# Kernel tuning notes

Measured on AMD Instinct MI355X. Metric: run time of the kernel, lower is better.

The kernel has to match this reference:

```python
import jax, jax.numpy as jnp
import numpy as np


def setup_inputs() -> dict:
    key = jax.random.key(0)
    ks = jax.random.split(key, 8)
    N, E, H, C, L, G = 100000, 1600000, 128, 10, 5, 64
    x = jax.random.normal(ks[0], (N, H), dtype=jnp.float32)
    edge_index = jax.random.randint(ks[1], (2, E), 0, N, dtype=jnp.int32)
    batch = jnp.sort(jax.random.randint(ks[2], (N,), 0, G, dtype=jnp.int32))
    # Glorot-ish init scale for stability
    Ws = jax.random.normal(ks[3], (L, H, H), dtype=jnp.float32) * (1.0 / np.sqrt(H))
    bs = jax.random.normal(ks[4], (L, H), dtype=jnp.float32) * 0.01
    W_out = jax.random.normal(ks[5], (H, C), dtype=jnp.float32) * (1.0 / np.sqrt(H))
    b_out = jax.random.normal(ks[6], (C,), dtype=jnp.float32) * 0.01
    return {"x": x, "edge_index": edge_index, "batch": batch, "num_graphs": G,
            "Ws": Ws, "bs": bs, "W_out": W_out, "b_out": b_out}


def reference(x, edge_index, batch, num_graphs, Ws, bs, W_out, b_out):
    N = x.shape[0]
    # --- GCN normalization (add self-loops, symmetric deg^-1/2 norm), computed once ---
    loop = jnp.arange(N, dtype=edge_index.dtype)
    src = jnp.concatenate([edge_index[0], loop])  # message sources (x_j)
    dst = jnp.concatenate([edge_index[1], loop])  # aggregation targets
    deg = jax.ops.segment_sum(jnp.ones_like(dst, dtype=x.dtype), dst, num_segments=N)
    dis = jnp.where(deg > 0, jax.lax.rsqrt(jnp.maximum(deg, 1.0)), 0.0)
    norm = dis[src] * dis[dst]  # [E+N]
    # --- stacked GCNConv + ReLU ---
    for l in range(Ws.shape[0]):
        xw = x @ Ws[l]                                   # [N, H] dense transform
        msg = norm[:, None] * xw[src]                    # gather + scale per edge
        x = jax.nn.relu(jax.ops.segment_sum(msg, dst, num_segments=N) + bs[l])
    # --- global mean pool over graphs ---
    sums = jax.ops.segment_sum(x, batch, num_segments=num_graphs)       # [G, H]
    cnts = jax.ops.segment_sum(jnp.ones((N,), x.dtype), batch, num_segments=num_graphs)
    pooled = sums / jnp.maximum(cnts, 1.0)[:, None]
    return pooled @ W_out + b_out
```

## Files before the change

kernel.cpp:

```cpp
#include <hip/hip_runtime.h>
#include <hip/hip_bf16.h>
#include <stdint.h>

#define HDIM 128

typedef __attribute__((ext_vector_type(8))) short short8;
typedef __attribute__((ext_vector_type(4))) float f32x4;

__device__ __forceinline__ ushort f2bf(float f) {
  uint u = __float_as_uint(f);
  u = (u + 0x7fffu + ((u >> 16) & 1u)) >> 16;
  return (ushort)u;
}
__device__ __forceinline__ float bflo(uint v) { return __uint_as_float(v << 16); }
__device__ __forceinline__ float bfhi(uint v) { return __uint_as_float(v & 0xffff0000u); }


__global__ __launch_bounds__(256) void bucket_edges(const int* __restrict__ ei,
                                                    int* __restrict__ cnt,
                                                    int* __restrict__ bktcur,
                                                    int2* __restrict__ bkt, int E,
                                                    float inv8, int cap) {
  __shared__ int hist[8], base[8];
  const int t = threadIdx.x;
  for (int i0 = blockIdx.x * 256; i0 < E; i0 += gridDim.x * 256) {
    int i = i0 + t;
    if (t < 8) hist[t] = 0;
    __syncthreads();
    int s = 0, d = 0, b = 0, rank = 0;
    bool valid = i < E;
    if (valid) {
      s = ei[i];
      d = ei[E + i];
      atomicAdd(&cnt[d], 1);
      b = min(7, (int)((float)d * inv8));
      rank = atomicAdd(&hist[b], 1);
    }
    __syncthreads();
    if (t < 8) base[t] = atomicAdd(&bktcur[t], hist[t]);
    __syncthreads();
    if (valid) bkt[(size_t)b * cap + base[b] + rank] = make_int2(s, d);
  }
}

__global__ __launch_bounds__(256) void dis_kernel(const int* __restrict__ cnt,
                                                  float* __restrict__ dis, int N) {
  int i = blockIdx.x * 256 + threadIdx.x;
  if (i < N) dis[i] = rsqrtf((float)(cnt[i] + 1));
}

__device__ __forceinline__ int pdeg4(int c) { return (c + 4) & ~3; }

__global__ __launch_bounds__(256) void scan1(const int* __restrict__ cnt,
                                             int* __restrict__ bsum, int N) {
  __shared__ int red[256];
  int b = blockIdx.x, t = threadIdx.x;
  int base = b * 1024;
  int s = 0;
  for (int i = t; i < 1024; i += 256) {
    int n = base + i;
    if (n < N) s += pdeg4(cnt[n]);
  }
  red[t] = s;
  __syncthreads();
  for (int off = 128; off; off >>= 1) {
    if (t < off) red[t] += red[t + off];
    __syncthreads();
  }
  if (t == 0) bsum[b] = red[0];
}

__global__ __launch_bounds__(256) void scan2(int* __restrict__ bsum, int nb) {
  __shared__ int sh[256];
  int t = threadIdx.x;
  int v = (t < nb) ? bsum[t] : 0;
  sh[t] = v;
  __syncthreads();
  for (int off = 1; off < 256; off <<= 1) {
    int add = (t >= off) ? sh[t - off] : 0;
    __syncthreads();
    sh[t] += add;
    __syncthreads();
  }
  if (t < nb) bsum[t] = sh[t] - v;
}

__global__ __launch_bounds__(256) void scan3(const int* __restrict__ cnt,
                                             const int* __restrict__ bsum,
                                             int* __restrict__ rowptr,
                                             int* __restrict__ cursor, int N) {
  __shared__ int sh[256];
  int b = blockIdx.x, t = threadIdx.x;
  int base = b * 1024 + t * 4;
  int v[4];
#pragma unroll
  for (int i = 0; i < 4; ++i) {
    int n = base + i;
    v[i] = (n < N) ? pdeg4(cnt[n]) : 0;
  }
  int tsum = v[0] + v[1] + v[2] + v[3];
  sh[t] = tsum;
  __syncthreads();
  for (int off = 1; off < 256; off <<= 1) {
    int add = (t >= off) ? sh[t - off] : 0;
    __syncthreads();
    sh[t] += add;
    __syncthreads();
  }
  int p = sh[t] - tsum + bsum[b];
#pragma unroll
  for (int i = 0; i < 4; ++i) {
    int n = base + i;
    if (n <= N) rowptr[n] = p;
    if (n < N) cursor[n] = p;
    p += v[i];
  }
}

__device__ __forceinline__ uint pack_cw(int src, float w) {
  uint w15 = (__float_as_uint(w) + 0x8000u) >> 16;
  return (uint)src | (w15 << 17);
}
__device__ __forceinline__ uint cw_src(uint u) { return u & 0x1FFFFu; }
__device__ __forceinline__ float cw_w(uint u) { return __uint_as_float((u >> 17) << 16); }

__global__ __launch_bounds__(256) void fill_csr2(const int2* __restrict__ bkt,
                                                 const int* __restrict__ bktcnt,
                                                 const float* __restrict__ dis,
                                                 int* __restrict__ cursor,
                                                 uint* __restrict__ colw, int cap,
                                                 int E, int N) {
  const int g = blockIdx.x & 7;
  const int nb = gridDim.x >> 3;
  const int bi = blockIdx.x >> 3;
  const int ecnt = bktcnt[g];
  const int2* eb = bkt + (size_t)g * cap;
  for (int i = bi * 256 + threadIdx.x; i < ecnt; i += nb * 256) {
    int2 sd = eb[i];
    int pos = atomicAdd(&cursor[sd.y], 1);
    colw[pos] = pack_cw(sd.x, dis[sd.x] * dis[sd.y]);
  }
  const int n0 = (g * N) >> 3, n1 = ((g + 1) * N) >> 3;
  for (int n = n0 + bi * 256 + threadIdx.x; n < n1; n += nb * 256) {
    int pos = atomicAdd(&cursor[n], 1);
    colw[pos] = pack_cw(n, dis[n] * dis[n]);
  }
}

__global__ __launch_bounds__(256) void pad_csr2(const int* __restrict__ cnt,
                                                const int* __restrict__ rowptr,
                                                uint* __restrict__ colw, int N) {
  const int g = blockIdx.x & 7;
  const int nb = gridDim.x >> 3;
  const int bi = blockIdx.x >> 3;
  const int n0 = (g * N) >> 3, n1 = ((g + 1) * N) >> 3;
  for (int n = n0 + bi * 256 + threadIdx.x; n < n1; n += nb * 256) {
    int beg = rowptr[n] + cnt[n] + 1, end = rowptr[n + 1];
    for (int j = beg; j < end; ++j) colw[j] = (uint)n;
  }
}

__global__ __launch_bounds__(256) void swz_w(const float* __restrict__ Ws,
                                             ushort* __restrict__ Wsw, int total) {
  int idx = blockIdx.x * 256 + threadIdx.x;
  if (idx >= total) return;
  int l = idx >> 14, r = idx & 16383;
  int j = r & 7, lane = (r >> 3) & 63, kk = (r >> 9) & 3, c = r >> 11;
  int n = c * 16 + (lane & 15);
  int k = kk * 32 + (lane >> 4) * 8 + j;
  Wsw[idx] = f2bf(Ws[l * 16384 + k * HDIM + n]);
}


template <bool F32IN>
__global__ __launch_bounds__(256) void gemm_kernel(const void* __restrict__ Xin,
                                                   const ushort* __restrict__ Wsw,
                                                   ushort* __restrict__ XW, int N,
                                                   int ntiles) {
  __shared__ ushort wlds[16384];
  __shared__ ushort clds[64 * 136];
  const int t = threadIdx.x;
  {
    const int4* src = (const int4*)Wsw;
    int4* dst = (int4*)wlds;
#pragma unroll
    for (int i = 0; i < 8; ++i) dst[t + 256 * i] = src[t + 256 * i];
  }
  __syncthreads();

  const int wave = t >> 6, lane = t & 63;
  const int kq = lane >> 4;

  for (int tile = blockIdx.x; tile < ntiles; tile += gridDim.x) {
    const int row0 = tile * 64 + wave * 16 + (lane & 15);
    const bool inb = row0 < N;

    short8 afr[4];
#pragma unroll
    for (int kk = 0; kk < 4; ++kk) afr[kk] = short8{0, 0, 0, 0, 0, 0, 0, 0};
    if (inb) {
      if constexpr (F32IN) {
        const float* arow = (const float*)Xin + (size_t)row0 * HDIM;
#pragma unroll
        for (int kk = 0; kk < 4; ++kk) {
          float4 x0 = *(const float4*)(arow + kk * 32 + kq * 8);
          float4 x1 = *(const float4*)(arow + kk * 32 + kq * 8 + 4);
          short8 f;
          f[0] = (short)f2bf(x0.x); f[1] = (short)f2bf(x0.y);
          f[2] = (short)f2bf(x0.z); f[3] = (short)f2bf(x0.w);
          f[4] = (short)f2bf(x1.x); f[5] = (short)f2bf(x1.y);
          f[6] = (short)f2bf(x1.z); f[7] = (short)f2bf(x1.w);
          afr[kk] = f;
        }
      } else {
        const short8* arow = (const short8*)((const ushort*)Xin + (size_t)row0 * HDIM);
#pragma unroll
        for (int kk = 0; kk < 4; ++kk) afr[kk] = arow[kk * 4 + kq];
      }
    }

    f32x4 acc[8];
#pragma unroll
    for (int c = 0; c < 8; ++c) acc[c] = f32x4{0.f, 0.f, 0.f, 0.f};
#pragma unroll
    for (int kk = 0; kk < 4; ++kk) {
#pragma unroll
      for (int c = 0; c < 8; ++c) {
        short8 bfr = *(const short8*)(wlds + (((c * 4 + kk) * 64 + lane) << 3));
        acc[c] = __builtin_amdgcn_mfma_f32_16x16x32_bf16(afr[kk], bfr, acc[c], 0, 0, 0);
      }
    }

    __syncthreads();
    const int m0 = wave * 16 + kq * 4;
#pragma unroll
    for (int c = 0; c < 8; ++c) {
      int col = c * 16 + (lane & 15);
#pragma unroll
      for (int r = 0; r < 4; ++r) clds[(m0 + r) * 136 + col] = f2bf(acc[c][r]);
    }
    __syncthreads();
#pragma unroll
    for (int i = 0; i < 4; ++i) {
      int idx = t + 256 * i;
      int row = idx >> 4, piece = idx & 15;
      int grow = tile * 64 + row;
      if (grow < N)
        ((int4*)XW)[(size_t)tile * 1024 + idx] =
            *(const int4*)(clds + row * 136 + piece * 8);
    }
  }
}

__global__ __launch_bounds__(256, 6) void agg_kernel(const ushort* __restrict__ XW,
                                                     const uint* __restrict__ colw,
                                                     const int* __restrict__ rowptr,
                                                     const float* __restrict__ bias,
                                                     ushort* __restrict__ Y, int N) {
  const int lane = threadIdx.x & 63;
  const int node = blockIdx.x * 4 + (threadIdx.x >> 6);
  if (node >= N) return;
  const int e = lane >> 4, c = lane & 15;
  const int beg = rowptr[node];
  const int pdeg = rowptr[node + 1] - beg;
  const int last = pdeg - 1;

  uint cw[6];
#pragma unroll
  for (int k = 0; k < 6; ++k) {
    int off = 4 * k + e;
    cw[k] = __builtin_nontemporal_load(colw + beg + (off < pdeg ? off : last));
  }
  uint4 gv[6];
#pragma unroll
  for (int k = 0; k < 6; ++k)
    gv[k] = *(const uint4*)(XW + ((size_t)cw_src(cw[k]) << 7) + c * 8);

  float acc[8];
#pragma unroll
  for (int i = 0; i < 8; ++i) acc[i] = 0.f;

#pragma unroll
  for (int k = 0; k < 6; ++k) {
    int off = 4 * k + e;
    float w = (off < pdeg) ? cw_w(cw[k]) : 0.f;
    uint4 v = gv[k];
    acc[0] += w * bflo(v.x); acc[1] += w * bfhi(v.x);
    acc[2] += w * bflo(v.y); acc[3] += w * bfhi(v.y);
    acc[4] += w * bflo(v.z); acc[5] += w * bfhi(v.z);
    acc[6] += w * bflo(v.w); acc[7] += w * bfhi(v.w);
  }
  for (int off = 24 + e; off < pdeg; off += 4) {
    uint u = __builtin_nontemporal_load(colw + beg + off);
    uint4 v = *(const uint4*)(XW + ((size_t)cw_src(u) << 7) + c * 8);
    float w = cw_w(u);
    acc[0] += w * bflo(v.x); acc[1] += w * bfhi(v.x);
    acc[2] += w * bflo(v.y); acc[3] += w * bfhi(v.y);
    acc[4] += w * bflo(v.z); acc[5] += w * bfhi(v.z);
    acc[6] += w * bflo(v.w); acc[7] += w * bfhi(v.w);
  }

#pragma unroll
  for (int i = 0; i < 8; ++i) {
    acc[i] += __shfl_xor(acc[i], 16, 64);
    acc[i] += __shfl_xor(acc[i], 32, 64);
  }
  if (e == 0) {
    float4 b0 = *(const float4*)(bias + c * 8);
    float4 b1 = *(const float4*)(bias + c * 8 + 4);
    uint4 pk;
    pk.x = (uint)f2bf(fmaxf(acc[0] + b0.x, 0.f)) | ((uint)f2bf(fmaxf(acc[1] + b0.y, 0.f)) << 16);
    pk.y = (uint)f2bf(fmaxf(acc[2] + b0.z, 0.f)) | ((uint)f2bf(fmaxf(acc[3] + b0.w, 0.f)) << 16);
    pk.z = (uint)f2bf(fmaxf(acc[4] + b1.x, 0.f)) | ((uint)f2bf(fmaxf(acc[5] + b1.y, 0.f)) << 16);
    pk.w = (uint)f2bf(fmaxf(acc[6] + b1.z, 0.f)) | ((uint)f2bf(fmaxf(acc[7] + b1.w, 0.f)) << 16);
    *(uint4*)(Y + (size_t)node * HDIM + c * 8) = pk;
  }
}


__global__ __launch_bounds__(256) void pool_partial(const ushort* __restrict__ x,
                                                    const int* __restrict__ batch,
                                                    float* __restrict__ pooled,
                                                    int* __restrict__ gcnt, int N) {
  const int g = blockIdx.x, s = blockIdx.y;
  const int t = threadIdx.x;
  __shared__ int range[2];
  __shared__ float sums[256];
  if (t < 2) {
    int target = g + t;
    int lo = 0, hi = N;
    while (lo < hi) {
      int mid = (lo + hi) >> 1;
      if (batch[mid] < target) lo = mid + 1;
      else hi = mid;
    }
    range[t] = lo;
  }
  __syncthreads();
  int beg = range[0], end = range[1];
  if (s == 0 && t == 0) gcnt[g] = end - beg;
  int col = t & 127, half = t >> 7;
  float acc = 0.f;
  for (int n = beg + s * 2 + half; n < end; n += 16) {
    acc += __uint_as_float(((uint)x[(size_t)n * HDIM + col]) << 16);
  }
  sums[t] = acc;
  __syncthreads();
  if (t < 128) atomicAdd(&pooled[g * HDIM + t], sums[t] + sums[t + 128]);
}

__global__ __launch_bounds__(256) void out_final(const float* __restrict__ pooled,
                                                 const int* __restrict__ gcnt,
                                                 const float* __restrict__ W_out,
                                                 const float* __restrict__ b_out,
                                                 float* __restrict__ out, int G, int C) {
  int i = blockIdx.x * 256 + threadIdx.x;
  if (i >= G * C) return;
  int g = i / C, c = i - g * C;
  float inv = 1.f / (float)max(gcnt[g], 1);
  const float* pg = pooled + g * HDIM;
  float o = 0.f;
  for (int h = 0; h < HDIM; ++h) o += pg[h] * W_out[h * C + c];
  out[i] = b_out[c] + o * inv;
}


extern "C" void kernel_launch(void* const* d_in, const int* in_sizes, int n_in,
                              void* d_out, int out_size, void* d_ws, size_t ws_size,
                              hipStream_t stream) {
  (void)n_in;
  (void)ws_size;
  const float* x = (const float*)d_in[0];
  const int* ei = (const int*)d_in[1];
  const int* batch = (const int*)d_in[2];
  const float* Ws = (const float*)d_in[4];
  const float* bs = (const float*)d_in[5];
  const float* W_out = (const float*)d_in[6];
  const float* b_out = (const float*)d_in[7];
  float* out = (float*)d_out;

  const int N = in_sizes[0] / HDIM;
  const int E = in_sizes[1] / 2;
  const int L = in_sizes[5] / HDIM;
  const int C = in_sizes[7];
  const int G = out_size / C;
  const int cap = E / 4 + 1024;

  char* p = (char*)d_ws;
  auto carve = [&](size_t bytes) {
    char* r = p;
    p += (bytes + 255) & ~(size_t)255;
    return r;
  };
  int* cnt = (int*)carve((size_t)N * 4);
  int* bktcur = (int*)carve(256);
  float* dis = (float*)carve((size_t)N * 4);
  int* rowptr = (int*)carve((size_t)(N + 1) * 4);
  int* cursor = (int*)carve((size_t)N * 4);
  int* bsum = (int*)carve(4096);
  int2* bkt = (int2*)carve((size_t)8 * cap * 8);
  uint* colw = (uint*)carve(((size_t)E + 4 * (size_t)N + 64) * 4);
  ushort* Wsw = (ushort*)carve((size_t)L * HDIM * HDIM * 2);
  ushort* xw = (ushort*)carve((size_t)N * HDIM * 2);
  ushort* y0 = (ushort*)carve((size_t)N * HDIM * 2);
  ushort* y1 = (ushort*)carve((size_t)N * HDIM * 2);
  float* pooled = (float*)carve((size_t)G * HDIM * 4 + (size_t)G * 4);
  int* gcnt = (int*)(pooled + (size_t)G * HDIM);

  hipMemsetAsync(cnt, 0, (size_t)N * 4, stream);
  hipMemsetAsync(bktcur, 0, 256, stream);
  hipMemsetAsync(pooled, 0, (size_t)G * HDIM * 4 + (size_t)G * 4, stream);

  const float inv8 = 8.0f / (float)N;
  bucket_edges<<<1024, 256, 0, stream>>>(ei, cnt, bktcur, bkt, E, inv8, cap);
  dis_kernel<<<(N + 255) / 256, 256, 0, stream>>>(cnt, dis, N);
  int nb = (N + 1 + 1023) / 1024;
  scan1<<<nb, 256, 0, stream>>>(cnt, bsum, N);
  scan2<<<1, 256, 0, stream>>>(bsum, nb);
  scan3<<<nb, 256, 0, stream>>>(cnt, bsum, rowptr, cursor, N);
  fill_csr2<<<1024, 256, 0, stream>>>(bkt, bktcur, dis, cursor, colw, cap, E, N);
  pad_csr2<<<1024, 256, 0, stream>>>(cnt, rowptr, colw, N);
  swz_w<<<(L * HDIM * HDIM + 255) / 256, 256, 0, stream>>>(Ws, Wsw, L * HDIM * HDIM);

  const int ntiles = (N + 63) / 64;
  const int gb = 768;
  gemm_kernel<true><<<gb, 256, 0, stream>>>(x, Wsw, xw, N, ntiles);
  agg_kernel<<<(N + 3) / 4, 256, 0, stream>>>(xw, colw, rowptr, bs, y0, N);
  ushort* xc = y0;
  ushort* xn = y1;
  for (int l = 1; l < L; ++l) {
    gemm_kernel<false><<<gb, 256, 0, stream>>>(xc, Wsw + (size_t)l * HDIM * HDIM, xw, N, ntiles);
    agg_kernel<<<(N + 3) / 4, 256, 0, stream>>>(xw, colw, rowptr, bs + (size_t)l * HDIM, xn, N);
    ushort* tmp = xc;
    xc = xn;
    xn = tmp;
  }
  pool_partial<<<dim3(G, 8), 256, 0, stream>>>(xc, batch, pooled, gcnt, N);
  out_final<<<(G * C + 255) / 256, 256, 0, stream>>>(pooled, gcnt, W_out, b_out, out, G, C);
}
```

Baseline: 664.0 us.

## Rewrite edge bucketing with wave ballots, packed 32-bit entries, and bucket-local degree counting

The edge bucketing kernel now ranks edges within each wavefront using ballots instead of shared-memory atomics and block barriers. It packs each edge as a local destination offset plus source into a single 32-bit word, which halves the bucket storage, and pads the per-bucket counters to separate cache lines. Degree counting moves into a new kernel that reads the buckets, so the global degree atomics land on a localized range. The cost is one extra launch and an extra pass over the bucket array. The packing relies on N being small enough that a source fits in 18 bits and a bucket-local offset fits in 14 bits.

```diff
diff --git a/kernel.cpp b/kernel.cpp
--- a/kernel.cpp
+++ b/kernel.cpp
@@ -17,29 +17,88 @@
 
 
 __global__ __launch_bounds__(256) void bucket_edges(const int* __restrict__ ei,
-                                                    int* __restrict__ cnt,
                                                     int* __restrict__ bktcur,
-                                                    int2* __restrict__ bkt, int E,
-                                                    float inv8, int cap) {
-  __shared__ int hist[8], base[8];
-  const int t = threadIdx.x;
-  for (int i0 = blockIdx.x * 256; i0 < E; i0 += gridDim.x * 256) {
-    int i = i0 + t;
-    if (t < 8) hist[t] = 0;
-    __syncthreads();
-    int s = 0, d = 0, b = 0, rank = 0;
-    bool valid = i < E;
+                                                    uint* __restrict__ bkt, int E,
+                                                    int N, float inv8, int cap) {
+  const int lane = threadIdx.x & 63;
+  const int wavei = blockIdx.x * 4 + (threadIdx.x >> 6);
+  const int base_idx = wavei * 256;
+  if (base_idx >= E) return;
+  const unsigned long long lt = (1ull << lane) - 1ull;
+
+  int bs[4], rk[4], pf[4];
+  uint pk[4];
+  int tot[8];
+#pragma unroll
+  for (int k = 0; k < 8; ++k) tot[k] = 0;
+
+#pragma unroll
+  for (int j = 0; j < 4; ++j) {
+    int idx = base_idx + j * 64 + lane;
+    bool valid = idx < E;
+    int b = 8;
     if (valid) {
-      s = ei[i];
-      d = ei[E + i];
-      atomicAdd(&cnt[d], 1);
-      b = min(7, (int)((float)d * inv8));
-      rank = atomicAdd(&hist[b], 1);
-    }
-    __syncthreads();
-    if (t < 8) base[t] = atomicAdd(&bktcur[t], hist[t]);
-    __syncthreads();
-    if (valid) bkt[(size_t)b * cap + base[b] + rank] = make_int2(s, d);
+      int s = ei[idx];
+      int d = ei[E + idx];
+      b = (int)((float)d * inv8);
+      int n0b = (b * N) >> 3;
+      if (d < n0b) {
+        --b;
+        n0b = (b * N) >> 3;
+      } else {
+        int n1b = ((b + 1) * N) >> 3;
+        if (d >= n1b) {
+          ++b;
+          n0b = n1b;
+        }
+      }
+      pk[j] = (uint)(d - n0b) | ((uint)s << 14);
+    }
+    int rank = 0, prefix = 0;
+#pragma unroll
+    for (int k = 0; k < 8; ++k) {
+      unsigned long long m = __ballot(b == k);
+      int c = __popcll(m);
+      if (b == k) {
+        rank = __popcll(m & lt);
+        prefix = tot[k];
+      }
+      tot[k] += c;
+    }
+    bs[j] = b;
+    rk[j] = rank;
+    pf[j] = prefix;
+  }
+
+  int myTot = 0;
+#pragma unroll
+  for (int k = 0; k < 8; ++k)
+    if (lane == k) myTot = tot[k];
+  int mybase = 0;
+  if (lane < 8 && myTot > 0) mybase = atomicAdd(&bktcur[lane * 16], myTot);
+#pragma unroll
+  for (int j = 0; j < 4; ++j) {
+    if (bs[j] < 8) {
+      int bb = __shfl(mybase, bs[j], 64);
+      __builtin_nontemporal_store(
+          pk[j], &bkt[(size_t)bs[j] * cap + bb + pf[j] + rk[j]]);
+    }
+  }
+}
+
+__global__ __launch_bounds__(256) void count_local(const uint* __restrict__ bkt,
+                                                   const int* __restrict__ bktcur,
+                                                   int* __restrict__ cnt, int cap,
+                                                   int N) {
+  const int g = blockIdx.x & 7;
+  const int nb = gridDim.x >> 3;
+  const int bi = blockIdx.x >> 3;
+  const int ecnt = bktcur[g * 16];
+  const int n0 = (g * N) >> 3;
+  const uint* eb = bkt + (size_t)g * cap;
+  for (int i = bi * 256 + threadIdx.x; i < ecnt; i += nb * 256) {
+    uint u = __builtin_nontemporal_load(eb + i);
+    atomicAdd(&cnt[n0 + (int)(u & 0x3FFFu)], 1);
   }
 }
 
@@ -124,23 +183,26 @@
 __device__ __forceinline__ uint cw_src(uint u) { return u & 0x1FFFFu; }
 __device__ __forceinline__ float cw_w(uint u) { return __uint_as_float((u >> 17) << 16); }
 
-__global__ __launch_bounds__(256) void fill_csr2(const int2* __restrict__ bkt,
-                                                 const int* __restrict__ bktcnt,
+__global__ __launch_bounds__(256) void fill_csr2(const uint* __restrict__ bkt,
+                                                 const int* __restrict__ bktcur,
                                                  const float* __restrict__ dis,
                                                  int* __restrict__ cursor,
                                                  uint* __restrict__ colw, int cap,
-                                                 int E, int N) {
+                                                 int N) {
   const int g = blockIdx.x & 7;
   const int nb = gridDim.x >> 3;
   const int bi = blockIdx.x >> 3;
-  const int ecnt = bktcnt[g];
-  const int2* eb = bkt + (size_t)g * cap;
+  const int ecnt = bktcur[g * 16];
+  const int n0 = (g * N) >> 3;
+  const uint* eb = bkt + (size_t)g * cap;
   for (int i = bi * 256 + threadIdx.x; i < ecnt; i += nb * 256) {
-    int2 sd = eb[i];
-    int pos = atomicAdd(&cursor[sd.y], 1);
-    colw[pos] = pack_cw(sd.x, dis[sd.x] * dis[sd.y]);
-  }
-  const int n0 = (g * N) >> 3, n1 = ((g + 1) * N) >> 3;
+    uint u = __builtin_nontemporal_load(eb + i);
+    int d = n0 + (int)(u & 0x3FFFu);
+    int s = (int)(u >> 14);
+    int pos = atomicAdd(&cursor[d], 1);
+    colw[pos] = pack_cw(s, dis[s] * dis[d]);
+  }
+  const int n1 = ((g + 1) * N) >> 3;
   for (int n = n0 + bi * 256 + threadIdx.x; n < n1; n += nb * 256) {
     int pos = atomicAdd(&cursor[n], 1);
     colw[pos] = pack_cw(n, dis[n] * dis[n]);
@@ -393,12 +455,12 @@
     return r;
   };
   int* cnt = (int*)carve((size_t)N * 4);
-  int* bktcur = (int*)carve(256);
+  int* bktcur = (int*)carve(512);
   float* dis = (float*)carve((size_t)N * 4);
   int* rowptr = (int*)carve((size_t)(N + 1) * 4);
   int* cursor = (int*)carve((size_t)N * 4);
   int* bsum = (int*)carve(4096);
-  int2* bkt = (int2*)carve((size_t)8 * cap * 8);
+  uint* bkt = (uint*)carve((size_t)8 * cap * 4);
   uint* colw = (uint*)carve(((size_t)E + 4 * (size_t)N + 64) * 4);
   ushort* Wsw = (ushort*)carve((size_t)L * HDIM * HDIM * 2);
   ushort* xw = (ushort*)carve((size_t)N * HDIM * 2);
@@ -408,17 +470,18 @@
   int* gcnt = (int*)(pooled + (size_t)G * HDIM);
 
   hipMemsetAsync(cnt, 0, (size_t)N * 4, stream);
-  hipMemsetAsync(bktcur, 0, 256, stream);
+  hipMemsetAsync(bktcur, 0, 512, stream);
   hipMemsetAsync(pooled, 0, (size_t)G * HDIM * 4 + (size_t)G * 4, stream);
 
   const float inv8 = 8.0f / (float)N;
-  bucket_edges<<<1024, 256, 0, stream>>>(ei, cnt, bktcur, bkt, E, inv8, cap);
+  bucket_edges<<<(E + 1023) / 1024, 256, 0, stream>>>(ei, bktcur, bkt, E, N, inv8, cap);
+  count_local<<<1024, 256, 0, stream>>>(bkt, bktcur, cnt, cap, N);
   dis_kernel<<<(N + 255) / 256, 256, 0, stream>>>(cnt, dis, N);
   int nb = (N + 1 + 1023) / 1024;
   scan1<<<nb, 256, 0, stream>>>(cnt, bsum, N);
   scan2<<<1, 256, 0, stream>>>(bsum, nb);
   scan3<<<nb, 256, 0, stream>>>(cnt, bsum, rowptr, cursor, N);
-  fill_csr2<<<1024, 256, 0, stream>>>(bkt, bktcur, dis, cursor, colw, cap, E, N);
+  fill_csr2<<<1024, 256, 0, stream>>>(bkt, bktcur, dis, cursor, colw, cap, N);
   pad_csr2<<<1024, 256, 0, stream>>>(cnt, rowptr, colw, N);
   swz_w<<<(L * HDIM * HDIM + 255) / 256, 256, 0, stream>>>(Ws, Wsw, L * HDIM * HDIM);
 
```

New measurement: 761.3 us. 14.7% more time.
